# Performance work log

Hardware: AMD Instinct MI355X
Metric: run time of the kernel (lower is better)

Reference implementation:

```python
import jax, jax.numpy as jnp
import numpy as np

D_MODEL = 1024
N_HEADS = 16
D_K = D_MODEL // N_HEADS


def setup_inputs() -> dict:
    key = jax.random.key(0)
    k1, k2, k3 = jax.random.split(key, 3)
    x = jax.random.normal(k1, (4, 2048, D_MODEL), dtype=jnp.float32)
    # torch nn.Linear(d_model, 3*d_model, bias=False): y = x @ W.T, W: [3D, D].
    # We store transposed weights [D, 3D] so y = x @ W_attn (same math).
    scale = 1.0 / np.sqrt(D_MODEL)
    W_attn = jax.random.uniform(k2, (D_MODEL, 3 * D_MODEL), dtype=jnp.float32, minval=-scale, maxval=scale)
    W_proj = jax.random.uniform(k3, (D_MODEL, D_MODEL), dtype=jnp.float32, minval=-scale, maxval=scale)
    return {"x": x, "W_attn": W_attn, "W_proj": W_proj}


def reference(x, W_attn, W_proj):
    B, S, D = x.shape
    qkv = x @ W_attn                       # [B, S, 3D]
    q, k, v = jnp.split(qkv, 3, axis=-1)   # each [B, S, D]
    # [B, S, D] -> [B, H, S, d_k]
    def heads(t):
        return t.reshape(B, S, N_HEADS, D_K).transpose(0, 2, 1, 3)
    q, k, v = heads(q), heads(k), heads(v)
    scores = jnp.einsum('bhqd,bhkd->bhqk', q, k) / jnp.sqrt(jnp.float32(D_K))
    weights = jax.nn.softmax(scores, axis=-1)
    attn = jnp.einsum('bhqk,bhkd->bhqd', weights, v)  # [B, H, S, d_k]
    attn = attn.transpose(0, 2, 1, 3).reshape(B, S, D)
    return attn @ W_proj
```

## Files before the change

### kernel.cpp

```cpp
#include <hip/hip_runtime.h>
#include <hip/hip_bf16.h>

#define D_MODEL 1024
#define N_HEADS 16
#define SEQ     2048
#define BATCH   4
#define CSC     (0.125f * 1.44269504f)

typedef __attribute__((ext_vector_type(8))) short short8;
typedef __attribute__((ext_vector_type(4))) float f32x4;

__device__ __forceinline__ ushort f2bf(float v) {
    __hip_bfloat16 b = __float2bfloat16(v);
    return __builtin_bit_cast(ushort, b);
}
__device__ __forceinline__ f32x4 mfma16(short8 a, short8 b, f32x4 c) {
    return __builtin_amdgcn_mfma_f32_16x16x32_bf16(a, b, c, 0, 0, 0);
}
__device__ __forceinline__ void gload_lds16(const ushort* g, ushort* l) {
    __builtin_amdgcn_global_load_lds(
        (const __attribute__((address_space(1))) unsigned int*)g,
        (__attribute__((address_space(3))) unsigned int*)l, 16, 0, 0);
}

__global__ __launch_bounds__(256) void prep_k(const float* __restrict__ x,
                                              const float* __restrict__ Wa,
                                              const float* __restrict__ Wp,
                                              ushort* __restrict__ xh,
                                              ushort* __restrict__ WaT,
                                              ushort* __restrict__ WpT) {
    const int id = blockIdx.x;
    const int t = threadIdx.x;
    if (id < 2048) {
        const float4* x4 = (const float4*)x;
        ushort4* xh4 = (ushort4*)xh;
        const int n4 = BATCH * SEQ * D_MODEL / 4;
        for (int i = id * 256 + t; i < n4; i += 2048 * 256) {
            float4 v = x4[i];
            ushort4 hv;
            hv.x = f2bf(v.x);
            hv.y = f2bf(v.y);
            hv.z = f2bf(v.z);
            hv.w = f2bf(v.w);
            xh4[i] = hv;
        }
    } else {
        __shared__ float tile[32][33];
        const float* W;
        ushort* WT;
        int N, tid, scaleQ;
        if (id < 2048 + 3072) { tid = id - 2048; W = Wa; WT = WaT; N = 3072; scaleQ = 1; }
        else                  { tid = id - 5120; W = Wp; WT = WpT; N = 1024; scaleQ = 0; }
        const int nb = (tid % (N / 32)) * 32, kb = (tid / (N / 32)) * 32;
        const int tx = t & 31, ty = t >> 5;
#pragma unroll
        for (int i = 0; i < 4; ++i)
            tile[ty + 8 * i][tx] = W[(size_t)(kb + ty + 8 * i) * N + nb + tx];
        __syncthreads();
#pragma unroll
        for (int i = 0; i < 4; ++i) {
            int n = nb + ty + 8 * i;
            float v = tile[tx][ty + 8 * i];
            if (scaleQ && n < 1024) v *= CSC;
            WT[(size_t)n * 1024 + kb + tx] = f2bf(v);
        }
    }
}

__global__ __launch_bounds__(256) void transpose_v_k(const ushort* __restrict__ qkv_h,
                                                     ushort* __restrict__ vT_h) {
    __shared__ ushort th[64][68];
    const int st = blockIdx.x, h = blockIdx.y, b = blockIdx.z;
    const int t = threadIdx.x;
    const int s0 = st * 64;
    {
        int s = t >> 2, dc = (t & 3) * 16;
        const size_t src = ((size_t)(b * SEQ + s0 + s)) * 3072 + 2048 + h * 64 + dc;
        *(uint4*)&th[s][dc]     = *(const uint4*)&qkv_h[src];
        *(uint4*)&th[s][dc + 8] = *(const uint4*)&qkv_h[src + 8];
    }
    __syncthreads();
    {
        int d = t >> 2, sc = (t & 3) * 16;
        ushort bufh[16];
#pragma unroll
        for (int j = 0; j < 16; ++j) bufh[j] = th[sc + j][d];
        const size_t dst = ((size_t)((b * 16 + h) * 64 + d)) * SEQ + s0 + sc;
        *(uint4*)&vT_h[dst]     = *(uint4*)&bufh[0];
        *(uint4*)&vT_h[dst + 8] = *(uint4*)&bufh[8];
    }
}

template <int OUT_SPLIT>
__global__ __launch_bounds__(256) void gemm_k(
    const ushort* __restrict__ Ah, int lda, int aoff,
    const ushort* __restrict__ BhT,
    ushort* __restrict__ Ch, float* __restrict__ Cf,
    int ldc, int coff, int K) {
    __shared__ __align__(16) ushort lds[2][2][4096];
    const int t = threadIdx.x;
    const int lane = t & 63, wid = t >> 6;
    const int wm = (wid >> 1) * 64, wn = (wid & 1) * 64;
    const int row0 = blockIdx.y * 128, col0 = blockIdx.x * 128;

    f32x4 acc[4][4];
#pragma unroll
    for (int i = 0; i < 4; ++i)
#pragma unroll
        for (int j = 0; j < 4; ++j) acc[i][j] = f32x4{0.f, 0.f, 0.f, 0.f};

    const int r_loc = lane >> 2;
    const int c_src = (lane & 3) ^ ((lane >> 3) & 3);
    const int swz = ((lane & 15) >> 1) & 3;
    const int ch = (((lane >> 4) ^ swz) * 8);
    const int rA = wm + (lane & 15);
    const int rB = wn + (lane & 15);

    auto stage = [&](int buf, int kk) {
#pragma unroll
        for (int ic = 0; ic < 4; ++ic) {
            const int c = wid * 4 + ic;
            const int tile = c >> 3, chi = c & 7;
            const ushort* s = tile ? BhT : Ah;
            const int sr = tile ? col0 : row0;
            const int sl = tile ? K : lda;
            const int so = tile ? 0 : aoff;
            const ushort* gp =
                s + (size_t)(sr + chi * 16 + r_loc) * sl + so + kk + c_src * 8;
            gload_lds16(gp, &lds[buf][tile][chi * 512 + 0]);
        }
    };

    stage(0, 0);
    for (int k0 = 0; k0 < K; k0 += 32) {
        const int cur = (k0 >> 5) & 1;
        if (k0 + 32 < K) {
            stage(cur ^ 1, k0 + 32);
            asm volatile("s_waitcnt vmcnt(4)" ::: "memory");
        } else {
            asm volatile("s_waitcnt vmcnt(0)" ::: "memory");
        }
        __builtin_amdgcn_s_barrier();
        __builtin_amdgcn_sched_barrier(0);

        short8 ah[4], bh[4];
#pragma unroll
        for (int f = 0; f < 4; ++f) {
            ah[f] = *(const short8*)&lds[cur][0][(rA + f * 16) * 32 + ch];
            bh[f] = *(const short8*)&lds[cur][1][(rB + f * 16) * 32 + ch];
        }
        __builtin_amdgcn_s_setprio(1);
#pragma unroll
        for (int i = 0; i < 4; ++i)
#pragma unroll
            for (int j = 0; j < 4; ++j) acc[i][j] = mfma16(ah[i], bh[j], acc[i][j]);
        __builtin_amdgcn_s_setprio(0);
        asm volatile("s_waitcnt lgkmcnt(0)" ::: "memory");
        __builtin_amdgcn_s_barrier();
        __builtin_amdgcn_sched_barrier(0);
    }
#pragma unroll
    for (int i = 0; i < 4; ++i)
#pragma unroll
        for (int j = 0; j < 4; ++j)
#pragma unroll
            for (int r = 0; r < 4; ++r) {
                int row = row0 + wm + i * 16 + (lane >> 4) * 4 + r;
                int col = col0 + wn + j * 16 + (lane & 15);
                float v = acc[i][j][r];
                if (OUT_SPLIT) {
                    Ch[(size_t)row * ldc + coff + col] = f2bf(v);
                } else {
                    Cf[(size_t)row * ldc + coff + col] = v;
                }
            }
}

__global__ __launch_bounds__(512) void flash_mfma(
    const ushort* __restrict__ qkv_h, const ushort* __restrict__ vT_h,
    ushort* __restrict__ attn_h) {
    const int id = blockIdx.x;
    const int bh = id & 63, qt = id >> 6;
    const int h = bh & 15, b = bh >> 4;
    const int t = threadIdx.x, lane = t & 63, wid = t >> 6;
    const int q = lane & 15, g = lane >> 4;
    const int qs7 = q & 7;

    __shared__ __align__(16) ushort Kb[2][4096];
    __shared__ __align__(16) ushort Vb[4096];
    __shared__ __align__(16) ushort Pb[8][1024];

    const size_t tokbase = (size_t)b * SEQ;
    const int q0 = qt * 128;
    const int kv_r = lane >> 3;
    const int kv_csrc = (lane & 7) ^ ((lane >> 3) & 7);
    const size_t vbase = ((size_t)(b * 16 + h) * 64) * SEQ;

    ushort* KQ = &Kb[0][0];
#pragma unroll
    for (int is = 0; is < 2; ++is) {
        int ci = wid * 2 + is;
        const ushort* gq =
            qkv_h + (tokbase + q0 + ci * 8 + kv_r) * 3072 + h * 64 + kv_csrc * 8;
        gload_lds16(gq, KQ + ci * 512);
    }
    __syncthreads();
    const int ck0 = (g ^ qs7) * 8;
    const int ck1 = ((g + 4) ^ qs7) * 8;
    short8 qh[2];
    {
        const int row = wid * 16 + q;
        qh[0] = *(const short8*)&KQ[row * 64 + ck0];
        qh[1] = *(const short8*)&KQ[row * 64 + ck1];
    }
    __syncthreads();

    const int qck0 = q * 64 + ck0;
    const int qck1 = q * 64 + ck1;
    ushort* Pw = &Pb[wid][0];
    const int pw0 = q * 64 + (((g >> 1) + 0) ^ qs7) * 8 + (g & 1) * 4;
    const int pw1 = q * 64 + (((g >> 1) + 2) ^ qs7) * 8 + (g & 1) * 4;
    const int pw2 = q * 64 + (((g >> 1) + 4) ^ qs7) * 8 + (g & 1) * 4;
    const int pw3 = q * 64 + (((g >> 1) + 6) ^ qs7) * 8 + (g & 1) * 4;

    auto stageK = [&](int buf, int kv0) {
        const ushort* gsrc =
            qkv_h + (tokbase + kv0 + wid * 16) * 3072 + 1024 + h * 64;
        ushort* dst = &Kb[buf][wid * 1024];
#pragma unroll
        for (int is = 0; is < 2; ++is)
            gload_lds16(gsrc + (size_t)(is * 8 + kv_r) * 3072 + kv_csrc * 8,
                        dst + is * 512);
    };
    auto stageV = [&](int kv0) {
        const ushort* gsrc = vT_h + vbase + (size_t)((wid - 4) * 16) * SEQ + kv0;
        ushort* dst = &Vb[(wid - 4) * 1024];
#pragma unroll
        for (int is = 0; is < 2; ++is)
            gload_lds16(gsrc + (size_t)(is * 8 + kv_r) * SEQ + kv_csrc * 8,
                        dst + is * 512);
    };

    if (wid < 4) stageK(0, 0); else stageV(0);

    float l_ = 0.f;
    f32x4 o[4];
#pragma unroll
    for (int i = 0; i < 4; ++i) o[i] = f32x4{0.f, 0.f, 0.f, 0.f};

    auto body = [&](int cur) {
        const ushort* Kc = &Kb[cur][0];

        f32x4 s[4];
#pragma unroll
        for (int j = 0; j < 4; ++j) s[j] = f32x4{0.f, 0.f, 0.f, 0.f};
        __builtin_amdgcn_s_setprio(1);
#pragma unroll
        for (int j = 0; j < 4; ++j) {
            short8 kh0 = *(const short8*)&Kc[j * 1024 + qck0];
            s[j] = mfma16(kh0, qh[0], s[j]);
            short8 kh1 = *(const short8*)&Kc[j * 1024 + qck1];
            s[j] = mfma16(kh1, qh[1], s[j]);
        }
        __builtin_amdgcn_s_setprio(0);

        float rs = 0.f;
#pragma unroll
        for (int j = 0; j < 4; ++j) {
            ushort4 hv;
            float p0 = __builtin_exp2f(s[j][0]);
            float p1 = __builtin_exp2f(s[j][1]);
            float p2 = __builtin_exp2f(s[j][2]);
            float p3 = __builtin_exp2f(s[j][3]);
            rs += (p0 + p1) + (p2 + p3);
            hv.x = f2bf(p0);
            hv.y = f2bf(p1);
            hv.z = f2bf(p2);
            hv.w = f2bf(p3);
            const int off = (j == 0) ? pw0 : (j == 1) ? pw1 : (j == 2) ? pw2 : pw3;
            *(ushort4*)&Pw[off] = hv;
        }
        l_ += rs;
        asm volatile("s_waitcnt lgkmcnt(0)" ::: "memory");
        __builtin_amdgcn_sched_barrier(0);

        __builtin_amdgcn_s_setprio(1);
#pragma unroll
        for (int ks = 0; ks < 2; ++ks) {
            short8 pa = *(const short8*)&Pw[ks ? qck1 : qck0];
#pragma unroll
            for (int jp = 0; jp < 4; ++jp) {
                short8 vh = *(const short8*)&Vb[jp * 1024 + (ks ? qck1 : qck0)];
                o[jp] = mfma16(pa, vh, o[jp]);
            }
        }
        __builtin_amdgcn_s_setprio(0);

        asm volatile("s_waitcnt lgkmcnt(0)" ::: "memory");
        __builtin_amdgcn_s_barrier();
        __builtin_amdgcn_sched_barrier(0);
    };

    for (int kt2 = 0; kt2 < SEQ / 128; ++kt2) {
        if (wid < 4) {
            stageK(1, (kt2 * 2 + 1) * 64);
            asm volatile("s_waitcnt vmcnt(2)" ::: "memory");
        } else {
            asm volatile("s_waitcnt vmcnt(0)" ::: "memory");
        }
        __builtin_amdgcn_s_barrier();
        __builtin_amdgcn_sched_barrier(0);
        body(0);
        if (wid >= 4) stageV((kt2 * 2 + 1) * 64);
        if (wid < 4) {
            if (kt2 < SEQ / 128 - 1) {
                stageK(0, (kt2 * 2 + 2) * 64);
                asm volatile("s_waitcnt vmcnt(2)" ::: "memory");
            } else {
                asm volatile("s_waitcnt vmcnt(0)" ::: "memory");
            }
        } else {
            asm volatile("s_waitcnt vmcnt(0)" ::: "memory");
        }
        __builtin_amdgcn_s_barrier();
        __builtin_amdgcn_sched_barrier(0);
        body(1);
        if (wid >= 4 && kt2 < SEQ / 128 - 1) stageV((kt2 * 2 + 2) * 64);
    }

    l_ += __shfl_xor(l_, 16);
    l_ += __shfl_xor(l_, 32);
    float inv = 1.f / l_;
#pragma unroll
    for (int r = 0; r < 4; ++r) {
        float invr = __shfl(inv, (g << 2) + r);
        int tok = q0 + wid * 16 + g * 4 + r;
        size_t rowb = (tokbase + tok) * 3072;
#pragma unroll
        for (int jp = 0; jp < 4; ++jp) {
            int col = h * 64 + jp * 16 + q;
            attn_h[rowb + col] = f2bf(o[jp][r] * invr);
        }
    }
}


extern "C" void kernel_launch(void* const* d_in, const int* in_sizes, int n_in,
                              void* d_out, int out_size, void* d_ws, size_t ws_size,
                              hipStream_t stream) {
    const float* x      = (const float*)d_in[0];
    const float* W_attn = (const float*)d_in[1];
    const float* W_proj = (const float*)d_in[2];

    const int M = BATCH * SEQ;

    ushort* qkv_h = (ushort*)d_ws;
    ushort* WaT   = qkv_h + (size_t)M * 3072;
    ushort* WpT   = WaT + (size_t)3072 * 1024;

    ushort* xh   = (ushort*)d_out;
    ushort* vT_h = (ushort*)d_out;

    prep_k<<<dim3(6144), 256, 0, stream>>>(x, W_attn, W_proj, xh, WaT, WpT);
    gemm_k<1><<<dim3(24, 64), 256, 0, stream>>>(xh, 1024, 0, WaT,
                                                qkv_h, nullptr, 3072, 0, 1024);
    transpose_v_k<<<dim3(32, 16, 4), 256, 0, stream>>>(qkv_h, vT_h);
    flash_mfma<<<dim3(1024), 512, 0, stream>>>(qkv_h, vT_h, qkv_h + 2048);
    gemm_k<0><<<dim3(8, 64), 256, 0, stream>>>(qkv_h, 3072, 2048, WpT,
                                               nullptr, (float*)d_out, 1024, 0,
                                               1024);
}
```

Measured before the change: 225.7 us.

## Fuse V transpose into QKV GEMM epilogue and double-buffer V in flash kernel

Removes the separate V transpose kernel by having the QKV GEMM epilogue also write V columns into a transposed buffer placed in the workspace. The flash attention kernel now double-buffers V in LDS and stages K and V together one tile ahead, unifying the wait/barrier pattern. This saves a kernel launch and a read/write pass over V, at the cost of strided, uncoalesced 2-byte stores in the GEMM epilogue, extra LDS, and extra workspace usage.

```diff
diff --git a/kernel.cpp b/kernel.cpp
--- a/kernel.cpp
+++ b/kernel.cpp
@@ -67,35 +67,11 @@
     }
 }
 
-__global__ __launch_bounds__(256) void transpose_v_k(const ushort* __restrict__ qkv_h,
-                                                     ushort* __restrict__ vT_h) {
-    __shared__ ushort th[64][68];
-    const int st = blockIdx.x, h = blockIdx.y, b = blockIdx.z;
-    const int t = threadIdx.x;
-    const int s0 = st * 64;
-    {
-        int s = t >> 2, dc = (t & 3) * 16;
-        const size_t src = ((size_t)(b * SEQ + s0 + s)) * 3072 + 2048 + h * 64 + dc;
-        *(uint4*)&th[s][dc]     = *(const uint4*)&qkv_h[src];
-        *(uint4*)&th[s][dc + 8] = *(const uint4*)&qkv_h[src + 8];
-    }
-    __syncthreads();
-    {
-        int d = t >> 2, sc = (t & 3) * 16;
-        ushort bufh[16];
-#pragma unroll
-        for (int j = 0; j < 16; ++j) bufh[j] = th[sc + j][d];
-        const size_t dst = ((size_t)((b * 16 + h) * 64 + d)) * SEQ + s0 + sc;
-        *(uint4*)&vT_h[dst]     = *(uint4*)&bufh[0];
-        *(uint4*)&vT_h[dst + 8] = *(uint4*)&bufh[8];
-    }
-}
-
-template <int OUT_SPLIT>
+template <int OUT_SPLIT, int VT_FUSE>
 __global__ __launch_bounds__(256) void gemm_k(
     const ushort* __restrict__ Ah, int lda, int aoff,
     const ushort* __restrict__ BhT,
-    ushort* __restrict__ Ch, float* __restrict__ Cf,
+    ushort* __restrict__ Ch, float* __restrict__ Cf, ushort* __restrict__ vT,
     int ldc, int coff, int K) {
     __shared__ __align__(16) ushort lds[2][2][4096];
     const int t = threadIdx.x;
@@ -159,6 +135,7 @@
         __builtin_amdgcn_s_barrier();
         __builtin_amdgcn_sched_barrier(0);
     }
+    const bool isV = VT_FUSE && (col0 >= 2048);
 #pragma unroll
     for (int i = 0; i < 4; ++i)
 #pragma unroll
@@ -169,7 +146,13 @@
                 int col = col0 + wn + j * 16 + (lane & 15);
                 float v = acc[i][j][r];
                 if (OUT_SPLIT) {
-                    Ch[(size_t)row * ldc + coff + col] = f2bf(v);
+                    ushort hv = f2bf(v);
+                    Ch[(size_t)row * ldc + coff + col] = hv;
+                    if (isV) {
+                        int hd = col - 2048;
+                        int bb = row >> 11, s = row & 2047;
+                        vT[((size_t)(bb << 10) + hd) * SEQ + s] = hv;
+                    }
                 } else {
                     Cf[(size_t)row * ldc + coff + col] = v;
                 }
@@ -187,7 +170,7 @@
     const int qs7 = q & 7;
 
     __shared__ __align__(16) ushort Kb[2][4096];
-    __shared__ __align__(16) ushort Vb[4096];
+    __shared__ __align__(16) ushort Vb[2][4096];
     __shared__ __align__(16) ushort Pb[8][1024];
 
     const size_t tokbase = (size_t)b * SEQ;
@@ -223,25 +206,26 @@
     const int pw2 = q * 64 + (((g >> 1) + 4) ^ qs7) * 8 + (g & 1) * 4;
     const int pw3 = q * 64 + (((g >> 1) + 6) ^ qs7) * 8 + (g & 1) * 4;
 
-    auto stageK = [&](int buf, int kv0) {
-        const ushort* gsrc =
-            qkv_h + (tokbase + kv0 + wid * 16) * 3072 + 1024 + h * 64;
-        ushort* dst = &Kb[buf][wid * 1024];
-#pragma unroll
-        for (int is = 0; is < 2; ++is)
-            gload_lds16(gsrc + (size_t)(is * 8 + kv_r) * 3072 + kv_csrc * 8,
-                        dst + is * 512);
+    auto stage = [&](int buf, int kv0) {
+        if (wid < 4) {
+            const ushort* gsrc =
+                qkv_h + (tokbase + kv0 + wid * 16) * 3072 + 1024 + h * 64;
+            ushort* dst = &Kb[buf][wid * 1024];
+#pragma unroll
+            for (int is = 0; is < 2; ++is)
+                gload_lds16(gsrc + (size_t)(is * 8 + kv_r) * 3072 + kv_csrc * 8,
+                            dst + is * 512);
+        } else {
+            const ushort* gsrc = vT_h + vbase + (size_t)((wid - 4) * 16) * SEQ + kv0;
+            ushort* dst = &Vb[buf][(wid - 4) * 1024];
+#pragma unroll
+            for (int is = 0; is < 2; ++is)
+                gload_lds16(gsrc + (size_t)(is * 8 + kv_r) * SEQ + kv_csrc * 8,
+                            dst + is * 512);
+        }
     };
-    auto stageV = [&](int kv0) {
-        const ushort* gsrc = vT_h + vbase + (size_t)((wid - 4) * 16) * SEQ + kv0;
-        ushort* dst = &Vb[(wid - 4) * 1024];
-#pragma unroll
-        for (int is = 0; is < 2; ++is)
-            gload_lds16(gsrc + (size_t)(is * 8 + kv_r) * SEQ + kv_csrc * 8,
-                        dst + is * 512);
-    };
-
-    if (wid < 4) stageK(0, 0); else stageV(0);
+
+    stage(0, 0);
 
     float l_ = 0.f;
     f32x4 o[4];
@@ -250,6 +234,7 @@
 
     auto body = [&](int cur) {
         const ushort* Kc = &Kb[cur][0];
+        const ushort* Vc = &Vb[cur][0];
 
         f32x4 s[4];
 #pragma unroll
@@ -290,7 +275,7 @@
             short8 pa = *(const short8*)&Pw[ks ? qck1 : qck0];
 #pragma unroll
             for (int jp = 0; jp < 4; ++jp) {
-                short8 vh = *(const short8*)&Vb[jp * 1024 + (ks ? qck1 : qck0)];
+                short8 vh = *(const short8*)&Vc[jp * 1024 + (ks ? qck1 : qck0)];
                 o[jp] = mfma16(pa, vh, o[jp]);
             }
         }
@@ -302,30 +287,20 @@
     };
 
     for (int kt2 = 0; kt2 < SEQ / 128; ++kt2) {
-        if (wid < 4) {
-            stageK(1, (kt2 * 2 + 1) * 64);
+        stage(1, (kt2 * 2 + 1) * 64);
+        asm volatile("s_waitcnt vmcnt(2)" ::: "memory");
+        __builtin_amdgcn_s_barrier();
+        __builtin_amdgcn_sched_barrier(0);
+        body(0);
+        if (kt2 < SEQ / 128 - 1) {
+            stage(0, (kt2 * 2 + 2) * 64);
             asm volatile("s_waitcnt vmcnt(2)" ::: "memory");
         } else {
             asm volatile("s_waitcnt vmcnt(0)" ::: "memory");
         }
         __builtin_amdgcn_s_barrier();
         __builtin_amdgcn_sched_barrier(0);
-        body(0);
-        if (wid >= 4) stageV((kt2 * 2 + 1) * 64);
-        if (wid < 4) {
-            if (kt2 < SEQ / 128 - 1) {
-                stageK(0, (kt2 * 2 + 2) * 64);
-                asm volatile("s_waitcnt vmcnt(2)" ::: "memory");
-            } else {
-                asm volatile("s_waitcnt vmcnt(0)" ::: "memory");
-            }
-        } else {
-            asm volatile("s_waitcnt vmcnt(0)" ::: "memory");
-        }
-        __builtin_amdgcn_s_barrier();
-        __builtin_amdgcn_sched_barrier(0);
         body(1);
-        if (wid >= 4 && kt2 < SEQ / 128 - 1) stageV((kt2 * 2 + 2) * 64);
     }
 
     l_ += __shfl_xor(l_, 16);
@@ -357,16 +332,16 @@
     ushort* qkv_h = (ushort*)d_ws;
     ushort* WaT   = qkv_h + (size_t)M * 3072;
     ushort* WpT   = WaT + (size_t)3072 * 1024;
-
-    ushort* xh   = (ushort*)d_out;
-    ushort* vT_h = (ushort*)d_out;
+    ushort* vT_h  = WpT + (size_t)1024 * 1024;
+
+    ushort* xh = (ushort*)d_out;
 
     prep_k<<<dim3(6144), 256, 0, stream>>>(x, W_attn, W_proj, xh, WaT, WpT);
-    gemm_k<1><<<dim3(24, 64), 256, 0, stream>>>(xh, 1024, 0, WaT,
-                                                qkv_h, nullptr, 3072, 0, 1024);
-    transpose_v_k<<<dim3(32, 16, 4), 256, 0, stream>>>(qkv_h, vT_h);
+    gemm_k<1, 1><<<dim3(24, 64), 256, 0, stream>>>(xh, 1024, 0, WaT,
+                                                   qkv_h, nullptr, vT_h,
+                                                   3072, 0, 1024);
     flash_mfma<<<dim3(1024), 512, 0, stream>>>(qkv_h, vT_h, qkv_h + 2048);
-    gemm_k<0><<<dim3(8, 64), 256, 0, stream>>>(qkv_h, 3072, 2048, WpT,
-                                               nullptr, (float*)d_out, 1024, 0,
-                                               1024);
-}
+    gemm_k<0, 0><<<dim3(8, 64), 256, 0, stream>>>(qkv_h, 3072, 2048, WpT,
+                                                  nullptr, (float*)d_out, nullptr,
+                                                  1024, 0, 1024);
+}
```

Measured after the change: 235.2 us. 4.2% more time.

## Double-buffer V in flash attention and remap GEMM workgroups for locality

Applied to the files above, without the earlier changes.

The flash attention kernel now double-buffers V in LDS just like K, so K and V loads for the next tile are issued together and overlap with compute. Previously V had one buffer and its load could only start after the current body finished. The GEMM kernel also remaps workgroup IDs in an interleaved pattern so that concurrently scheduled blocks share operand tiles, aiming at better cache reuse. vT_h moves from the output buffer into the workspace, which needs more workspace memory and increases LDS use per block.

```diff
diff --git a/kernel.cpp b/kernel.cpp
--- a/kernel.cpp
+++ b/kernel.cpp
@@ -101,7 +101,12 @@
     const int t = threadIdx.x;
     const int lane = t & 63, wid = t >> 6;
     const int wm = (wid >> 1) * 64, wn = (wid & 1) * 64;
-    const int row0 = blockIdx.y * 128, col0 = blockIdx.x * 128;
+
+    const int gx = gridDim.x;
+    const int nwg = gx * gridDim.y;
+    const int flat = blockIdx.y * gx + blockIdx.x;
+    const int swzid = (flat & 7) * (nwg >> 3) + (flat >> 3);
+    const int row0 = (swzid / gx) * 128, col0 = (swzid % gx) * 128;
 
     f32x4 acc[4][4];
 #pragma unroll
@@ -187,7 +192,7 @@
     const int qs7 = q & 7;
 
     __shared__ __align__(16) ushort Kb[2][4096];
-    __shared__ __align__(16) ushort Vb[4096];
+    __shared__ __align__(16) ushort Vb[2][4096];
     __shared__ __align__(16) ushort Pb[8][1024];
 
     const size_t tokbase = (size_t)b * SEQ;
@@ -223,25 +228,26 @@
     const int pw2 = q * 64 + (((g >> 1) + 4) ^ qs7) * 8 + (g & 1) * 4;
     const int pw3 = q * 64 + (((g >> 1) + 6) ^ qs7) * 8 + (g & 1) * 4;
 
-    auto stageK = [&](int buf, int kv0) {
-        const ushort* gsrc =
-            qkv_h + (tokbase + kv0 + wid * 16) * 3072 + 1024 + h * 64;
-        ushort* dst = &Kb[buf][wid * 1024];
-#pragma unroll
-        for (int is = 0; is < 2; ++is)
-            gload_lds16(gsrc + (size_t)(is * 8 + kv_r) * 3072 + kv_csrc * 8,
-                        dst + is * 512);
+    auto stage = [&](int buf, int kv0) {
+        if (wid < 4) {
+            const ushort* gsrc =
+                qkv_h + (tokbase + kv0 + wid * 16) * 3072 + 1024 + h * 64;
+            ushort* dst = &Kb[buf][wid * 1024];
+#pragma unroll
+            for (int is = 0; is < 2; ++is)
+                gload_lds16(gsrc + (size_t)(is * 8 + kv_r) * 3072 + kv_csrc * 8,
+                            dst + is * 512);
+        } else {
+            const ushort* gsrc = vT_h + vbase + (size_t)((wid - 4) * 16) * SEQ + kv0;
+            ushort* dst = &Vb[buf][(wid - 4) * 1024];
+#pragma unroll
+            for (int is = 0; is < 2; ++is)
+                gload_lds16(gsrc + (size_t)(is * 8 + kv_r) * SEQ + kv_csrc * 8,
+                            dst + is * 512);
+        }
     };
-    auto stageV = [&](int kv0) {
-        const ushort* gsrc = vT_h + vbase + (size_t)((wid - 4) * 16) * SEQ + kv0;
-        ushort* dst = &Vb[(wid - 4) * 1024];
-#pragma unroll
-        for (int is = 0; is < 2; ++is)
-            gload_lds16(gsrc + (size_t)(is * 8 + kv_r) * SEQ + kv_csrc * 8,
-                        dst + is * 512);
-    };
-
-    if (wid < 4) stageK(0, 0); else stageV(0);
+
+    stage(0, 0);
 
     float l_ = 0.f;
     f32x4 o[4];
@@ -250,6 +256,7 @@
 
     auto body = [&](int cur) {
         const ushort* Kc = &Kb[cur][0];
+        const ushort* Vc = &Vb[cur][0];
 
         f32x4 s[4];
 #pragma unroll
@@ -290,7 +297,7 @@
             short8 pa = *(const short8*)&Pw[ks ? qck1 : qck0];
 #pragma unroll
             for (int jp = 0; jp < 4; ++jp) {
-                short8 vh = *(const short8*)&Vb[jp * 1024 + (ks ? qck1 : qck0)];
+                short8 vh = *(const short8*)&Vc[jp * 1024 + (ks ? qck1 : qck0)];
                 o[jp] = mfma16(pa, vh, o[jp]);
             }
         }
@@ -302,30 +309,20 @@
     };
 
     for (int kt2 = 0; kt2 < SEQ / 128; ++kt2) {
-        if (wid < 4) {
-            stageK(1, (kt2 * 2 + 1) * 64);
+        stage(1, (kt2 * 2 + 1) * 64);
+        asm volatile("s_waitcnt vmcnt(2)" ::: "memory");
+        __builtin_amdgcn_s_barrier();
+        __builtin_amdgcn_sched_barrier(0);
+        body(0);
+        if (kt2 < SEQ / 128 - 1) {
+            stage(0, (kt2 * 2 + 2) * 64);
             asm volatile("s_waitcnt vmcnt(2)" ::: "memory");
         } else {
             asm volatile("s_waitcnt vmcnt(0)" ::: "memory");
         }
         __builtin_amdgcn_s_barrier();
         __builtin_amdgcn_sched_barrier(0);
-        body(0);
-        if (wid >= 4) stageV((kt2 * 2 + 1) * 64);
-        if (wid < 4) {
-            if (kt2 < SEQ / 128 - 1) {
-                stageK(0, (kt2 * 2 + 2) * 64);
-                asm volatile("s_waitcnt vmcnt(2)" ::: "memory");
-            } else {
-                asm volatile("s_waitcnt vmcnt(0)" ::: "memory");
-            }
-        } else {
-            asm volatile("s_waitcnt vmcnt(0)" ::: "memory");
-        }
-        __builtin_amdgcn_s_barrier();
-        __builtin_amdgcn_sched_barrier(0);
         body(1);
-        if (wid >= 4 && kt2 < SEQ / 128 - 1) stageV((kt2 * 2 + 2) * 64);
     }
 
     l_ += __shfl_xor(l_, 16);
@@ -357,9 +354,9 @@
     ushort* qkv_h = (ushort*)d_ws;
     ushort* WaT   = qkv_h + (size_t)M * 3072;
     ushort* WpT   = WaT + (size_t)3072 * 1024;
-
-    ushort* xh   = (ushort*)d_out;
-    ushort* vT_h = (ushort*)d_out;
+    ushort* vT_h  = WpT + (size_t)1024 * 1024;
+
+    ushort* xh = (ushort*)d_out;
 
     prep_k<<<dim3(6144), 256, 0, stream>>>(x, W_attn, W_proj, xh, WaT, WpT);
     gemm_k<1><<<dim3(24, 64), 256, 0, stream>>>(xh, 1024, 0, WaT,
```

After: 217.3 us. 1.04x faster.
